# Kernel tuning notes

Hardware: AMD Instinct MI355X
Metric: run time of the kernel (lower is better)

## Reference

```python
import jax, jax.numpy as jnp
import numpy as np

EMBED = 4096
NUM_Q = 32
NUM_KV = 8
GROUPS = NUM_Q // NUM_KV  # 4
HEAD_DIM = EMBED // NUM_Q  # 128
KV_DIM = HEAD_DIM * NUM_KV  # 1024


def setup_inputs() -> dict:
    key = jax.random.key(0)
    ks = jax.random.split(key, 12)
    B, S = 2, 2048
    s = 0.02
    return {
        "query": jax.random.normal(ks[0], (B, S, EMBED), jnp.float32),
        "key": jax.random.normal(ks[1], (B, S, EMBED), jnp.float32),
        "value": jax.random.normal(ks[2], (B, S, EMBED), jnp.float32),
        # weights stored [in, out] (i.e. torch weight transposed)
        "Wq": jax.random.normal(ks[3], (EMBED, EMBED), jnp.float32) * s,
        "bq": jnp.zeros((EMBED,), jnp.float32),
        "Wk": jax.random.normal(ks[4], (EMBED, KV_DIM), jnp.float32) * s,
        "bk": jnp.zeros((KV_DIM,), jnp.float32),
        "Wv": jax.random.normal(ks[5], (EMBED, KV_DIM), jnp.float32) * s,
        "bv": jnp.zeros((KV_DIM,), jnp.float32),
        "Wo": jax.random.normal(ks[6], (EMBED, EMBED), jnp.float32) * s,
        "bo": jnp.zeros((EMBED,), jnp.float32),
    }


def reference(query, key, value, Wq, bq, Wk, bk, Wv, bv, Wo, bo):
    B, S, _ = query.shape
    Q = query @ Wq + bq                      # [B,S,E]
    K = key @ Wk + bk                        # [B,S,KV_DIM]
    V = value @ Wv + bv                      # [B,S,KV_DIM]
    # Q head h attends kv head h // GROUPS (repeat_interleave semantics):
    # reshape Q heads as (kv_head, group)
    Q = Q.reshape(B, S, NUM_KV, GROUPS, HEAD_DIM).transpose(0, 2, 3, 1, 4)  # [B,Hkv,G,S,D]
    K = K.reshape(B, S, NUM_KV, HEAD_DIM).transpose(0, 2, 1, 3)             # [B,Hkv,S,D]
    V = V.reshape(B, S, NUM_KV, HEAD_DIM).transpose(0, 2, 1, 3)             # [B,Hkv,S,D]
    scale = 1.0 / jnp.sqrt(jnp.asarray(HEAD_DIM, query.dtype))
    scores = jnp.einsum('bhgqd,bhkd->bhgqk', Q, K) * scale  # [B,Hkv,G,S,S]
    w = jax.nn.softmax(scores, axis=-1)
    y = jnp.einsum('bhgqk,bhkd->bhgqd', w, V)                # [B,Hkv,G,S,D]
    # back to [B,S,E] with head order (kv_head*GROUPS + group)
    y = y.transpose(0, 3, 1, 2, 4).reshape(B, S, EMBED)
    return y @ Wo + bo  # dropout is identity in eval mode
```

## Files before the change

kernel.cpp:

```cpp
#include <hip/hip_runtime.h>

typedef unsigned short u16;
typedef __attribute__((ext_vector_type(8))) short s16x8;
typedef __attribute__((ext_vector_type(4))) short s16x4;
typedef __attribute__((ext_vector_type(4))) float f32x4;

#define DEVI static __device__ __forceinline__

constexpr int BATCH = 2;
constexpr int SEQ   = 2048;
constexpr int EMB   = 4096;
constexpr int NQ    = 32;
constexpr int NKV   = 8;
constexpr int HD    = 128;
constexpr int KVD   = 1024;
constexpr int MR    = BATCH * SEQ;


DEVI u16 f2bf(float f) {
  union { float f; unsigned u; } x; x.f = f;
  unsigned r = x.u + 0x7FFFu + ((x.u >> 16) & 1u);
  return (u16)(r >> 16);
}

DEVI void mfma_acc(f32x4& c, s16x8 a, s16x8 b) {
  asm volatile("v_mfma_f32_16x16x32_bf16 %0, %1, %2, %0" : "+v"(c) : "v"(a), "v"(b));
}

DEVI void gload16(const void* g, void* l) {
  __builtin_amdgcn_global_load_lds(
      (const __attribute__((address_space(1))) void*)g,
      (__attribute__((address_space(3))) void*)l, 16, 0, 0);
}

DEVI float fexp2(float x) {
#if __has_builtin(__builtin_amdgcn_exp2f)
  return __builtin_amdgcn_exp2f(x);
#else
  return exp2f(x);
#endif
}

DEVI void store_out(u16* C, size_t idx, float v)   { C[idx] = f2bf(v); }
DEVI void store_out(float* C, size_t idx, float v) { C[idx] = v; }


__global__ __launch_bounds__(256) void cvt_f32_bf16(const float* __restrict__ in,
                                                    u16* __restrict__ out, int n8) {
  int i = blockIdx.x * 256 + threadIdx.x;
  if (i >= n8) return;
  const float4* p4 = (const float4*)in;
  float4 a = p4[2 * (size_t)i], b = p4[2 * (size_t)i + 1];
  u16 t[8];
  t[0] = f2bf(a.x); t[1] = f2bf(a.y); t[2] = f2bf(a.z); t[3] = f2bf(a.w);
  t[4] = f2bf(b.x); t[5] = f2bf(b.y); t[6] = f2bf(b.z); t[7] = f2bf(b.w);
  *(s16x8*)(out + 8 * (size_t)i) = *(const s16x8*)t;
}


__global__ __launch_bounds__(256) void transp_cvt(const float* __restrict__ W,
                                                  u16* __restrict__ Wt,
                                                  int Kd, int Nd) {
  __shared__ u16 tile[32][33];
  int tx = threadIdx.x, ty = threadIdx.y;
  int n0 = blockIdx.x * 32, k0 = blockIdx.y * 32;
#pragma unroll
  for (int j = 0; j < 4; ++j)
    tile[ty + 8 * j][tx] = f2bf(W[(size_t)(k0 + ty + 8 * j) * Nd + n0 + tx]);
  __syncthreads();
#pragma unroll
  for (int j = 0; j < 4; ++j)
    Wt[(size_t)(n0 + ty + 8 * j) * Kd + k0 + tx] = tile[tx][ty + 8 * j];
}


__global__ __launch_bounds__(256) void transp_v(const u16* __restrict__ Vp,
                                                u16* __restrict__ Vt) {
  __shared__ u16 tile[32][33];
  int tx = threadIdx.x, ty = threadIdx.y;
  int bh = blockIdx.z, b = bh >> 3, h = bh & 7;
  int s0 = blockIdx.x * 32, d0 = blockIdx.y * 32;
  const u16* src = Vp + (size_t)b * SEQ * KVD + h * HD;
#pragma unroll
  for (int j = 0; j < 4; ++j)
    tile[ty + 8 * j][tx] = src[(size_t)(s0 + ty + 8 * j) * KVD + d0 + tx];
  __syncthreads();
  u16* dst = Vt + (size_t)bh * HD * SEQ;
#pragma unroll
  for (int j = 0; j < 4; ++j)
    dst[(size_t)(d0 + ty + 8 * j) * SEQ + s0 + tx] = tile[tx][ty + 8 * j];
}


template <typename OT>
__global__ __launch_bounds__(256) void gemm_bt(const u16* __restrict__ A,
                                               const u16* __restrict__ Bt,
                                               const float* __restrict__ bias,
                                               OT* __restrict__ C,
                                               int M, int N, int K) {
  __shared__ __align__(16) u16 As[128 * 32];
  __shared__ __align__(16) u16 Bs[128 * 32];
  const int tid = threadIdx.x;
  const int lane = tid & 63, w = tid >> 6;
  const int wr = w >> 1, wc = w & 1;
  const int l15 = lane & 15, g = lane >> 4;
  const int m0 = blockIdx.y * 128, n0 = blockIdx.x * 128;
  const int srow = lane >> 2, schunk = lane & 3;
  const int fsw = (srow ^ (srow >> 2)) & 3;
  const int fr  = (l15  ^ (l15  >> 2)) & 3;

  f32x4 acc[4][4] = {};

  const u16* Ag = A  + (size_t)(m0 + w * 32 + srow) * K + ((schunk ^ fsw) << 3);
  const u16* Bg = Bt + (size_t)(n0 + w * 32 + srow) * K + ((schunk ^ fsw) << 3);
  u16* Al = As + (w * 32) * 32;
  u16* Bl = Bs + (w * 32) * 32;

  for (int k0 = 0; k0 < K; k0 += 32) {
    __syncthreads();
    gload16(Ag + k0,                    Al);
    gload16(Ag + (size_t)16 * K + k0,   Al + 16 * 32);
    gload16(Bg + k0,                    Bl);
    gload16(Bg + (size_t)16 * K + k0,   Bl + 16 * 32);
    __syncthreads();

    s16x8 af[4], bfr[4];
#pragma unroll
    for (int rt = 0; rt < 4; ++rt)
      af[rt] = *(const s16x8*)(As + (wr * 64 + rt * 16 + l15) * 32 + ((g ^ fr) << 3));
#pragma unroll
    for (int ct = 0; ct < 4; ++ct)
      bfr[ct] = *(const s16x8*)(Bs + (wc * 64 + ct * 16 + l15) * 32 + ((g ^ fr) << 3));
#pragma unroll
    for (int rt = 0; rt < 4; ++rt)
#pragma unroll
      for (int ct = 0; ct < 4; ++ct)
        mfma_acc(acc[rt][ct], af[rt], bfr[ct]);
  }

#pragma unroll
  for (int ct = 0; ct < 4; ++ct) {
    const int col = n0 + wc * 64 + ct * 16 + l15;
    const float bv = bias[col];
#pragma unroll
    for (int rt = 0; rt < 4; ++rt) {
      const int row = m0 + wr * 64 + rt * 16 + g * 4;
#pragma unroll
      for (int i = 0; i < 4; ++i)
        store_out(C, (size_t)(row + i) * N + col, acc[rt][ct][i] + bv);
    }
  }
}


__global__ __launch_bounds__(256, 2) void attn(const u16* __restrict__ Q,
                                               const u16* __restrict__ Kp,
                                               const u16* __restrict__ Vt,
                                               u16* __restrict__ Y) {
  __shared__ __align__(16) u16 Kb[2][64 * 128];
  __shared__ __align__(16) u16 Vb[2][128 * 64];

  const int tid = threadIdx.x, lane = tid & 63, w = tid >> 6;
  const int l15 = lane & 15, g = lane >> 4;
  const int g0 = g & 1, g1 = g >> 1;
  const int bz = blockIdx.y, b = bz >> 5, qh = bz & 31, h = qh >> 2;
  const int q0 = blockIdx.x * 128;
  constexpr float C1 = 0.08838834764831845f * 1.4426950408889634f;

  s16x8 qf[2][4];
  const u16* qptr = Q + (size_t)(b * SEQ + q0 + w * 32) * EMB + qh * HD;
#pragma unroll
  for (int rt = 0; rt < 2; ++rt)
#pragma unroll
    for (int ks = 0; ks < 4; ++ks)
      qf[rt][ks] = *(const s16x8*)(qptr + (size_t)(rt * 16 + l15) * EMB + ks * 32 + g * 8);

  const u16* kbase = Kp + (size_t)b * SEQ * KVD + h * HD;
  const u16* vbase = Vt + (size_t)(b * NKV + h) * HD * SEQ;

  auto stage = [&](int buf, int kv0) {
#pragma unroll
    for (int p = 0; p < 4; ++p) {
      int r = p * 16 + w * 4 + (lane >> 4);
      const u16* src = kbase + (size_t)(kv0 + r) * KVD + (((lane & 15) ^ (r & 7)) << 3);
      gload16(src, &Kb[buf][p * 2048 + w * 512]);
    }
#pragma unroll
    for (int p = 0; p < 4; ++p) {
      int r = p * 32 + w * 8 + (lane >> 3);
      const u16* src = vbase + (size_t)r * SEQ + kv0 + (((lane & 7) ^ (r & 7)) << 3);
      gload16(src, &Vb[buf][p * 2048 + w * 512]);
    }
  };

  const int addrA = (((g0 << 5) | l15)) << 2;
  const int addrB = (((g0 << 5) | 16 | l15)) << 2;

  f32x4 o[2][8] = {};
  float m_[2] = {-1e30f, -1e30f}, l_[2] = {0.f, 0.f};

  stage(0, 0);
  __syncthreads();

  for (int t = 0; t < SEQ / 64; ++t) {
    const int cur = t & 1;
    if (t < SEQ / 64 - 1) stage(cur ^ 1, (t + 1) * 64);

    f32x4 sacc[2][4] = {};
    __builtin_amdgcn_s_setprio(1);
#pragma unroll
    for (int ks = 0; ks < 4; ++ks) {
      s16x8 kf[4];
#pragma unroll
      for (int ct = 0; ct < 4; ++ct) {
        const int blk = ((ks << 2) | g) ^ (l15 & 7);
        kf[ct] = *(const s16x8*)&Kb[cur][(ct * 16 + l15) * 128 + (blk << 3)];
      }
#pragma unroll
      for (int rt = 0; rt < 2; ++rt)
#pragma unroll
        for (int ct = 0; ct < 4; ++ct)
          mfma_acc(sacc[rt][ct], kf[ct], qf[rt][ks]);
    }
    __builtin_amdgcn_s_setprio(0);

    s16x8 pvf[2][2];
#pragma unroll
    for (int rt = 0; rt < 2; ++rt) {
      float mx = -1e30f;
#pragma unroll
      for (int ct = 0; ct < 4; ++ct)
#pragma unroll
        for (int i = 0; i < 4; ++i) mx = fmaxf(mx, sacc[rt][ct][i]);
      mx *= C1;
      mx = fmaxf(mx, __shfl_xor(mx, 16));
      mx = fmaxf(mx, __shfl_xor(mx, 32));
      const float mn = fmaxf(m_[rt], mx);
      const float al = fexp2(m_[rt] - mn);
      m_[rt] = mn;

      float rs = 0.f;
      int wd[4][2];
#pragma unroll
      for (int ct = 0; ct < 4; ++ct) {
        float p0 = fexp2(sacc[rt][ct][0] * C1 - mn);
        float p1 = fexp2(sacc[rt][ct][1] * C1 - mn);
        float p2 = fexp2(sacc[rt][ct][2] * C1 - mn);
        float p3 = fexp2(sacc[rt][ct][3] * C1 - mn);
        rs += (p0 + p1) + (p2 + p3);
        asm("v_cvt_pk_bf16_f32 %0, %1, %2" : "=v"(wd[ct][0]) : "v"(p0), "v"(p1));
        asm("v_cvt_pk_bf16_f32 %0, %1, %2" : "=v"(wd[ct][1]) : "v"(p2), "v"(p3));
      }
      rs += __shfl_xor(rs, 16);
      rs += __shfl_xor(rs, 32);
      l_[rt] = l_[rt] * al + rs;
#pragma unroll
      for (int dt = 0; dt < 8; ++dt) {
        o[rt][dt][0] *= al; o[rt][dt][1] *= al;
        o[rt][dt][2] *= al; o[rt][dt][3] *= al;
      }

#pragma unroll
      for (int ks2 = 0; ks2 < 2; ++ks2) {
        union { int w4[4]; s16x8 v; } u;
#pragma unroll
        for (int s = 0; s < 2; ++s) {
          const int c0 = wd[2 * ks2][s], c1 = wd[2 * ks2 + 1][s];
          const int r0 = __builtin_amdgcn_ds_bpermute(addrA, c0);
          const int r1 = __builtin_amdgcn_ds_bpermute(addrA, c1);
          u.w4[s] = g1 ? r1 : r0;
          const int r2 = __builtin_amdgcn_ds_bpermute(addrB, c0);
          const int r3 = __builtin_amdgcn_ds_bpermute(addrB, c1);
          u.w4[2 + s] = g1 ? r3 : r2;
        }
        pvf[rt][ks2] = u.v;
      }
    }

    __builtin_amdgcn_s_setprio(1);
#pragma unroll
    for (int ks2 = 0; ks2 < 2; ++ks2)
#pragma unroll
      for (int dt = 0; dt < 8; ++dt) {
        const int blk = ((ks2 << 2) | g) ^ (l15 & 7);
        const s16x8 vf = *(const s16x8*)&Vb[cur][(dt * 16 + l15) * 64 + (blk << 3)];
        mfma_acc(o[0][dt], vf, pvf[0][ks2]);
        mfma_acc(o[1][dt], vf, pvf[1][ks2]);
      }
    __builtin_amdgcn_s_setprio(0);

    __syncthreads();
  }

  u16* ybase = Y + (size_t)(b * SEQ + q0 + w * 32) * EMB + qh * HD;
#pragma unroll
  for (int rt = 0; rt < 2; ++rt) {
    const float inv = 1.f / l_[rt];
    u16* yr = ybase + (size_t)(rt * 16 + l15) * EMB + g * 4;
#pragma unroll
    for (int dt = 0; dt < 8; ++dt) {
      u16 t4[4];
#pragma unroll
      for (int i = 0; i < 4; ++i) t4[i] = f2bf(o[rt][dt][i] * inv);
      *(s16x4*)(yr + dt * 16) = *(const s16x4*)t4;
    }
  }
}


extern "C" void kernel_launch(void* const* d_in, const int* in_sizes, int n_in,
                              void* d_out, int out_size, void* d_ws, size_t ws_size,
                              hipStream_t stream) {
  (void)in_sizes; (void)n_in; (void)out_size;
  const float* q_in = (const float*)d_in[0];
  const float* k_in = (const float*)d_in[1];
  const float* v_in = (const float*)d_in[2];
  const float* Wq = (const float*)d_in[3];
  const float* bq = (const float*)d_in[4];
  const float* Wk = (const float*)d_in[5];
  const float* bk = (const float*)d_in[6];
  const float* Wv = (const float*)d_in[7];
  const float* bv = (const float*)d_in[8];
  const float* Wo = (const float*)d_in[9];
  const float* bo = (const float*)d_in[10];
  float* out = (float*)d_out;

  char* base = (char*)d_ws;
  size_t off = 0;
  auto alloc = [&](size_t bytes) -> void* {
    void* r = base + off;
    off += (bytes + 255) & ~(size_t)255;
    return r;
  };
  u16* qb  = (u16*)alloc((size_t)MR * EMB * 2);
  u16* kb  = (u16*)alloc((size_t)MR * EMB * 2);
  u16* vb  = (u16*)alloc((size_t)MR * EMB * 2);
  u16* Wqt = (u16*)alloc((size_t)EMB * EMB * 2);
  u16* Wkt = (u16*)alloc((size_t)KVD * EMB * 2);
  u16* Wvt = (u16*)alloc((size_t)KVD * EMB * 2);
  u16* Wot = (u16*)alloc((size_t)EMB * EMB * 2);
  u16* Qp  = (u16*)alloc((size_t)MR * EMB * 2);
  u16* Kpp = (u16*)alloc((size_t)MR * KVD * 2);
  u16* Vpp = (u16*)alloc((size_t)MR * KVD * 2);
  u16* Vtt = (u16*)alloc((size_t)MR * KVD * 2);
  u16* Y   = qb;
  if (off > ws_size) return;

  const int n8 = MR * EMB / 8;
  cvt_f32_bf16<<<n8 / 256, 256, 0, stream>>>(q_in, qb, n8);
  cvt_f32_bf16<<<n8 / 256, 256, 0, stream>>>(k_in, kb, n8);
  cvt_f32_bf16<<<n8 / 256, 256, 0, stream>>>(v_in, vb, n8);
  transp_cvt<<<dim3(EMB / 32, EMB / 32), dim3(32, 8), 0, stream>>>(Wq, Wqt, EMB, EMB);
  transp_cvt<<<dim3(KVD / 32, EMB / 32), dim3(32, 8), 0, stream>>>(Wk, Wkt, EMB, KVD);
  transp_cvt<<<dim3(KVD / 32, EMB / 32), dim3(32, 8), 0, stream>>>(Wv, Wvt, EMB, KVD);
  transp_cvt<<<dim3(EMB / 32, EMB / 32), dim3(32, 8), 0, stream>>>(Wo, Wot, EMB, EMB);

  gemm_bt<u16><<<dim3(EMB / 128, MR / 128), 256, 0, stream>>>(qb, Wqt, bq, Qp, MR, EMB, EMB);
  gemm_bt<u16><<<dim3(KVD / 128, MR / 128), 256, 0, stream>>>(kb, Wkt, bk, Kpp, MR, KVD, EMB);
  gemm_bt<u16><<<dim3(KVD / 128, MR / 128), 256, 0, stream>>>(vb, Wvt, bv, Vpp, MR, KVD, EMB);
  transp_v<<<dim3(SEQ / 32, HD / 32, BATCH * NKV), dim3(32, 8), 0, stream>>>(Vpp, Vtt);
  attn<<<dim3(SEQ / 128, BATCH * NQ), 256, 0, stream>>>(Qp, Kpp, Vtt, Y);
  gemm_bt<float><<<dim3(EMB / 128, MR / 128), 256, 0, stream>>>(Y, Wot, bo, out, MR, EMB, EMB);
}
```

Baseline: 789.5 us.

## Read V directly from global, lazy softmax rescale, permlane swaps, raise occupancy

Drops the LDS staging buffer for V and has each lane load its V fragments straight from global memory, which halves shared memory use so launch bounds can request 3 blocks per CU. The online softmax now rescales only when some lane's new max exceeds the running max by more than 8 (log2 units). The per-tile row-sum shuffles are deferred to the epilogue. The bpermute-based P fragment shuffle is replaced with v_permlane32/16_swap instructions. The risks are uncoalesced, un-reused V global reads on every iteration and possible register pressure from the higher occupancy target.

```diff
diff --git a/kernel.cpp b/kernel.cpp
--- a/kernel.cpp
+++ b/kernel.cpp
@@ -153,16 +153,14 @@
 }
 
 
-__global__ __launch_bounds__(256, 2) void attn(const u16* __restrict__ Q,
+__global__ __launch_bounds__(256, 3) void attn(const u16* __restrict__ Q,
                                                const u16* __restrict__ Kp,
                                                const u16* __restrict__ Vt,
                                                u16* __restrict__ Y) {
   __shared__ __align__(16) u16 Kb[2][64 * 128];
-  __shared__ __align__(16) u16 Vb[2][128 * 64];
 
   const int tid = threadIdx.x, lane = tid & 63, w = tid >> 6;
   const int l15 = lane & 15, g = lane >> 4;
-  const int g0 = g & 1, g1 = g >> 1;
   const int bz = blockIdx.y, b = bz >> 5, qh = bz & 31, h = qh >> 2;
   const int q0 = blockIdx.x * 128;
   constexpr float C1 = 0.08838834764831845f * 1.4426950408889634f;
@@ -176,35 +174,26 @@
       qf[rt][ks] = *(const s16x8*)(qptr + (size_t)(rt * 16 + l15) * EMB + ks * 32 + g * 8);
 
   const u16* kbase = Kp + (size_t)b * SEQ * KVD + h * HD;
-  const u16* vbase = Vt + (size_t)(b * NKV + h) * HD * SEQ;
-
-  auto stage = [&](int buf, int kv0) {
+  const u16* vrow = Vt + (size_t)(b * NKV + h) * HD * SEQ + (size_t)l15 * SEQ + g * 8;
+
+  auto stageK = [&](int buf, int kv0) {
 #pragma unroll
     for (int p = 0; p < 4; ++p) {
       int r = p * 16 + w * 4 + (lane >> 4);
       const u16* src = kbase + (size_t)(kv0 + r) * KVD + (((lane & 15) ^ (r & 7)) << 3);
       gload16(src, &Kb[buf][p * 2048 + w * 512]);
     }
-#pragma unroll
-    for (int p = 0; p < 4; ++p) {
-      int r = p * 32 + w * 8 + (lane >> 3);
-      const u16* src = vbase + (size_t)r * SEQ + kv0 + (((lane & 7) ^ (r & 7)) << 3);
-      gload16(src, &Vb[buf][p * 2048 + w * 512]);
-    }
   };
-
-  const int addrA = (((g0 << 5) | l15)) << 2;
-  const int addrB = (((g0 << 5) | 16 | l15)) << 2;
 
   f32x4 o[2][8] = {};
   float m_[2] = {-1e30f, -1e30f}, l_[2] = {0.f, 0.f};
 
-  stage(0, 0);
+  stageK(0, 0);
   __syncthreads();
 
   for (int t = 0; t < SEQ / 64; ++t) {
     const int cur = t & 1;
-    if (t < SEQ / 64 - 1) stage(cur ^ 1, (t + 1) * 64);
+    if (t < SEQ / 64 - 1) stageK(cur ^ 1, (t + 1) * 64);
 
     f32x4 sacc[2][4] = {};
     __builtin_amdgcn_s_setprio(1);
@@ -227,51 +216,55 @@
     s16x8 pvf[2][2];
 #pragma unroll
     for (int rt = 0; rt < 2; ++rt) {
-      float mx = -1e30f;
-#pragma unroll
-      for (int ct = 0; ct < 4; ++ct)
-#pragma unroll
-        for (int i = 0; i < 4; ++i) mx = fmaxf(mx, sacc[rt][ct][i]);
-      mx *= C1;
-      mx = fmaxf(mx, __shfl_xor(mx, 16));
-      mx = fmaxf(mx, __shfl_xor(mx, 32));
-      const float mn = fmaxf(m_[rt], mx);
-      const float al = fexp2(m_[rt] - mn);
-      m_[rt] = mn;
+      float t0 = fmaxf(fmaxf(sacc[rt][0][0], sacc[rt][0][1]),
+                       fmaxf(sacc[rt][0][2], sacc[rt][0][3]));
+      float t1 = fmaxf(fmaxf(sacc[rt][1][0], sacc[rt][1][1]),
+                       fmaxf(sacc[rt][1][2], sacc[rt][1][3]));
+      float t2 = fmaxf(fmaxf(sacc[rt][2][0], sacc[rt][2][1]),
+                       fmaxf(sacc[rt][2][2], sacc[rt][2][3]));
+      float t3 = fmaxf(fmaxf(sacc[rt][3][0], sacc[rt][3][1]),
+                       fmaxf(sacc[rt][3][2], sacc[rt][3][3]));
+      const float pm = fmaxf(fmaxf(t0, t1), fmaxf(t2, t3)) * C1;
+
+      if (!__all(pm - m_[rt] <= 8.f)) {
+        float mr = pm;
+        mr = fmaxf(mr, __shfl_xor(mr, 16));
+        mr = fmaxf(mr, __shfl_xor(mr, 32));
+        const float mn = fmaxf(m_[rt], mr);
+        const float al = fexp2(m_[rt] - mn);
+        m_[rt] = mn;
+        l_[rt] *= al;
+#pragma unroll
+        for (int dt = 0; dt < 8; ++dt) {
+          o[rt][dt][0] *= al; o[rt][dt][1] *= al;
+          o[rt][dt][2] *= al; o[rt][dt][3] *= al;
+        }
+      }
+      const float mcur = m_[rt];
 
       float rs = 0.f;
       int wd[4][2];
 #pragma unroll
       for (int ct = 0; ct < 4; ++ct) {
-        float p0 = fexp2(sacc[rt][ct][0] * C1 - mn);
-        float p1 = fexp2(sacc[rt][ct][1] * C1 - mn);
-        float p2 = fexp2(sacc[rt][ct][2] * C1 - mn);
-        float p3 = fexp2(sacc[rt][ct][3] * C1 - mn);
+        float p0 = fexp2(sacc[rt][ct][0] * C1 - mcur);
+        float p1 = fexp2(sacc[rt][ct][1] * C1 - mcur);
+        float p2 = fexp2(sacc[rt][ct][2] * C1 - mcur);
+        float p3 = fexp2(sacc[rt][ct][3] * C1 - mcur);
         rs += (p0 + p1) + (p2 + p3);
         asm("v_cvt_pk_bf16_f32 %0, %1, %2" : "=v"(wd[ct][0]) : "v"(p0), "v"(p1));
         asm("v_cvt_pk_bf16_f32 %0, %1, %2" : "=v"(wd[ct][1]) : "v"(p2), "v"(p3));
       }
-      rs += __shfl_xor(rs, 16);
-      rs += __shfl_xor(rs, 32);
-      l_[rt] = l_[rt] * al + rs;
-#pragma unroll
-      for (int dt = 0; dt < 8; ++dt) {
-        o[rt][dt][0] *= al; o[rt][dt][1] *= al;
-        o[rt][dt][2] *= al; o[rt][dt][3] *= al;
-      }
+      l_[rt] += rs;
 
 #pragma unroll
       for (int ks2 = 0; ks2 < 2; ++ks2) {
         union { int w4[4]; s16x8 v; } u;
 #pragma unroll
         for (int s = 0; s < 2; ++s) {
-          const int c0 = wd[2 * ks2][s], c1 = wd[2 * ks2 + 1][s];
-          const int r0 = __builtin_amdgcn_ds_bpermute(addrA, c0);
-          const int r1 = __builtin_amdgcn_ds_bpermute(addrA, c1);
-          u.w4[s] = g1 ? r1 : r0;
-          const int r2 = __builtin_amdgcn_ds_bpermute(addrB, c0);
-          const int r3 = __builtin_amdgcn_ds_bpermute(addrB, c1);
-          u.w4[2 + s] = g1 ? r3 : r2;
+          int x = wd[2 * ks2][s], y = wd[2 * ks2 + 1][s];
+          asm volatile("v_permlane32_swap_b32 %0, %1" : "+v"(x), "+v"(y));
+          asm volatile("v_permlane16_swap_b32 %0, %1" : "+v"(x), "+v"(y));
+          u.w4[s] = x; u.w4[2 + s] = y;
         }
         pvf[rt][ks2] = u.v;
       }
@@ -282,8 +275,7 @@
     for (int ks2 = 0; ks2 < 2; ++ks2)
 #pragma unroll
       for (int dt = 0; dt < 8; ++dt) {
-        const int blk = ((ks2 << 2) | g) ^ (l15 & 7);
-        const s16x8 vf = *(const s16x8*)&Vb[cur][(dt * 16 + l15) * 64 + (blk << 3)];
+        const s16x8 vf = *(const s16x8*)(vrow + (size_t)dt * 16 * SEQ + t * 64 + ks2 * 32);
         mfma_acc(o[0][dt], vf, pvf[0][ks2]);
         mfma_acc(o[1][dt], vf, pvf[1][ks2]);
       }
@@ -295,7 +287,10 @@
   u16* ybase = Y + (size_t)(b * SEQ + q0 + w * 32) * EMB + qh * HD;
 #pragma unroll
   for (int rt = 0; rt < 2; ++rt) {
-    const float inv = 1.f / l_[rt];
+    float lt = l_[rt];
+    lt += __shfl_xor(lt, 16);
+    lt += __shfl_xor(lt, 32);
+    const float inv = 1.f / lt;
     u16* yr = ybase + (size_t)(rt * 16 + l15) * EMB + g * 4;
 #pragma unroll
     for (int dt = 0; dt < 8; ++dt) {
```

New measurement: 1.012 ms. 1.28x slower.
